# Optimization experiments

Hardware: AMD Instinct MI355X
Metric: run time of the kernel (lower is better)

The kernel has to match this reference:

```python
import jax, jax.numpy as jnp
import numpy as np

B = 2048
NUM_FEATURES = 40960
M = 256
N = 32
K = 32
MAX_EVAL = 10000.0  # Chess_Lib.MAX_EVAL stand-in
SPARSITY = 32.0 / NUM_FEATURES  # ~32 active HalfKP features per position


def _xavier(key, shape):
    fan_out, fan_in = shape
    limit = np.sqrt(6.0 / (fan_in + fan_out)).astype(np.float32)
    return jax.random.uniform(key, shape, jnp.float32, -limit, limit)


def setup_inputs() -> dict:
    key = jax.random.key(0)
    ks = jax.random.split(key, 8)
    # ~32-hot sparse binary feature vectors (HalfKP style)
    wf = (jax.random.uniform(ks[0], (B, NUM_FEATURES)) < SPARSITY).astype(jnp.float32)
    bf = (jax.random.uniform(ks[1], (B, NUM_FEATURES)) < SPARSITY).astype(jnp.float32)
    stm = jnp.round(jax.random.uniform(ks[2], (B, 1))).astype(jnp.float32)
    return {
        "white_features": wf,
        "black_features": bf,
        "stm": stm,
        "ft_w": _xavier(ks[3], (M, NUM_FEATURES)),
        "ft_b": jnp.zeros((M,), jnp.float32),
        "l1_w": _xavier(ks[4], (N, 2 * M)),
        "l1_b": jnp.zeros((N,), jnp.float32),
        "l2_w": _xavier(ks[5], (K, N)),
        "l2_b": jnp.zeros((K,), jnp.float32),
        "l3_w": _xavier(ks[6], (1, K)),
        "l3_b": jnp.zeros((1,), jnp.float32),
    }


def reference(white_features, black_features, stm, ft_w, ft_b,
              l1_w, l1_b, l2_w, l2_b, l3_w, l3_b):
    # feature transformer: [B,F] @ [F,M] -> [B,M]
    w = white_features @ ft_w.T + ft_b
    b = black_features @ ft_w.T + ft_b
    acc = stm * jnp.concatenate([w, b], axis=1) + (1.0 - stm) * jnp.concatenate([b, w], axis=1)
    l1_x = jnp.clip(acc, 0.0, 1.0)
    l2_x = jnp.clip(l1_x @ l1_w.T + l1_b, 0.0, 1.0)
    l3_x = jnp.clip(l2_x @ l2_w.T + l2_b, 0.0, 1.0)
    ev = jnp.clip(l3_x @ l3_w.T + l3_b, 0.0, 1.0)
    # align_eval without the python int() cast (kept batched/differentiable)
    return (ev - 0.5) * 2.0 * MAX_EVAL
```

## Files before the change

### kernel.cpp

```cpp
#include <hip/hip_runtime.h>
#include <hip/hip_bf16.h>

#define NF 40960
#define MD 256
#define BATCH 2048
#define NCHUNK 4
#define CHUNK (NF / NCHUNK)
#define CAPC 32

#define SCAN_BLOCKS (2 * BATCH * NCHUNK)
#define TRANS_BLOCKS ((NF / 64) * (MD / 64))

__device__ __forceinline__ float clip01(float v) {
    return fminf(fmaxf(v, 0.0f), 1.0f);
}

__global__ __launch_bounds__(256) void scan_transpose(
    const float* __restrict__ wf, const float* __restrict__ bfeat,
    const float* __restrict__ ft_w,
    float* __restrict__ ftT, int* __restrict__ g_cnt, int* __restrict__ g_idx)
{
    __shared__ float tile[64][65];
    __shared__ int s_cnt;
    __shared__ int s_idx[CAPC];

    const int b = blockIdx.x;
    const int t = threadIdx.x;

    if (b < SCAN_BLOCKS) {
        const int chunk = b & 3;
        const int pc    = b >> 2;
        const int color = pc & 1;
        const int pos   = pc >> 1;

        if (t == 0) s_cnt = 0;
        __syncthreads();

        const float* src = (color ? bfeat : wf) + (size_t)pos * NF + chunk * CHUNK;
        const float4* p4 = (const float4*)src;

        float4 v[10];
        #pragma unroll
        for (int k = 0; k < 10; ++k) v[k] = p4[t + 256 * k];

        #pragma unroll
        for (int k = 0; k < 10; ++k) {
            float4 a = v[k];
            if (a.x + a.y + a.z + a.w != 0.0f) {
                const int e = chunk * CHUNK + 4 * (t + 256 * k);
                if (a.x != 0.0f) { int q = atomicAdd(&s_cnt, 1); if (q < CAPC) s_idx[q] = e;     }
                if (a.y != 0.0f) { int q = atomicAdd(&s_cnt, 1); if (q < CAPC) s_idx[q] = e + 1; }
                if (a.z != 0.0f) { int q = atomicAdd(&s_cnt, 1); if (q < CAPC) s_idx[q] = e + 2; }
                if (a.w != 0.0f) { int q = atomicAdd(&s_cnt, 1); if (q < CAPC) s_idx[q] = e + 3; }
            }
        }
        __syncthreads();

        const int c = min(s_cnt, CAPC);
        if (t == 0) g_cnt[b] = c;
        if (t < c)  g_idx[(size_t)b * CAPC + t] = s_idx[t];
    } else {
        const int tb = b - SCAN_BLOCKS;
        const int f0 = (tb % (NF / 64)) * 64;
        const int m0 = (tb / (NF / 64)) * 64;
        const int tx = t & 63;
        const int ty = t >> 6;
        #pragma unroll
        for (int r = ty; r < 64; r += 4)
            tile[r][tx] = ft_w[(size_t)(m0 + r) * NF + f0 + tx];
        __syncthreads();
        #pragma unroll
        for (int r = ty; r < 64; r += 4)
            ftT[(size_t)(f0 + r) * MD + m0 + tx] = tile[tx][r];
    }
}

__global__ __launch_bounds__(256) void gather_mlp(
    const float* __restrict__ stm, const float* __restrict__ ftT,
    const int* __restrict__ g_cnt, const int* __restrict__ g_idx,
    const float* __restrict__ ft_b,
    const float* __restrict__ l1_w, const float* __restrict__ l1_b,
    const float* __restrict__ l2_w, const float* __restrict__ l2_b,
    const float* __restrict__ l3_w, const float* __restrict__ l3_b,
    float* __restrict__ out)
{
    __shared__ int lw[NCHUNK * CAPC], lb[NCHUNK * CAPC];
    __shared__ int cnts[8], offs[8];
    __shared__ int cw_s, cb_s;
    __shared__ float xsh[512];
    __shared__ float red[32][9];
    __shared__ float ysh[32], zsh[32];

    const int pos = blockIdx.x;
    const int t = threadIdx.x;

    if (t < 8) cnts[t] = g_cnt[(pos * 2 + (t >> 2)) * 4 + (t & 3)];
    __syncthreads();
    if (t == 0) {
        int ow = 0, ob = 0;
        #pragma unroll
        for (int c = 0; c < 4; ++c) {
            offs[c]     = ow; ow += cnts[c];
            offs[4 + c] = ob; ob += cnts[4 + c];
        }
        cw_s = ow; cb_s = ob;
    }
    __syncthreads();
    #pragma unroll
    for (int c = 0; c < 4; ++c) {
        if (t < cnts[c])     lw[offs[c] + t]     = g_idx[(size_t)((pos * 2 + 0) * 4 + c) * CAPC + t];
        if (t < cnts[4 + c]) lb[offs[4 + c] + t] = g_idx[(size_t)((pos * 2 + 1) * 4 + c) * CAPC + t];
    }
    __syncthreads();

    const int cw = cw_s, cb = cb_s;

    float accW = ft_b[t];
    float accB = ft_b[t];
    {
        int j = 0;
        for (; j + 4 <= cw; j += 4) {
            float a0 = ftT[(size_t)lw[j]     * MD + t];
            float a1 = ftT[(size_t)lw[j + 1] * MD + t];
            float a2 = ftT[(size_t)lw[j + 2] * MD + t];
            float a3 = ftT[(size_t)lw[j + 3] * MD + t];
            accW += a0 + a1 + a2 + a3;
        }
        for (; j < cw; ++j) accW += ftT[(size_t)lw[j] * MD + t];
        j = 0;
        for (; j + 4 <= cb; j += 4) {
            float a0 = ftT[(size_t)lb[j]     * MD + t];
            float a1 = ftT[(size_t)lb[j + 1] * MD + t];
            float a2 = ftT[(size_t)lb[j + 2] * MD + t];
            float a3 = ftT[(size_t)lb[j + 3] * MD + t];
            accB += a0 + a1 + a2 + a3;
        }
        for (; j < cb; ++j) accB += ftT[(size_t)lb[j] * MD + t];
    }

    const float s = stm[pos];
    xsh[t]       = clip01(s * accW + (1.0f - s) * accB);
    xsh[256 + t] = clip01(s * accB + (1.0f - s) * accW);
    __syncthreads();

    {
        const int n = t & 31;
        const int c = t >> 5;
        const float* w1 = l1_w + (size_t)n * 512 + c * 64;
        const float* xx = xsh + c * 64;
        float p = 0.0f;
        #pragma unroll
        for (int j = 0; j < 64; ++j) p += xx[j] * w1[j];
        red[n][c] = p;
    }
    __syncthreads();
    if (t < 32) {
        float v = l1_b[t];
        #pragma unroll
        for (int c = 0; c < 8; ++c) v += red[t][c];
        ysh[t] = clip01(v);
    }
    __syncthreads();

    if (t < 32) {
        float v = l2_b[t];
        const float* w2 = l2_w + t * 32;
        #pragma unroll
        for (int j = 0; j < 32; ++j) v += ysh[j] * w2[j];
        zsh[t] = clip01(v);
    }
    __syncthreads();

    if (t == 0) {
        float v = l3_b[0];
        #pragma unroll
        for (int j = 0; j < 32; ++j) v += zsh[j] * l3_w[j];
        v = clip01(v);
        out[pos] = (v - 0.5f) * 20000.0f;
    }
}

extern "C" void kernel_launch(void* const* d_in, const int* in_sizes, int n_in,
                              void* d_out, int out_size, void* d_ws, size_t ws_size,
                              hipStream_t stream) {
    const float* wf    = (const float*)d_in[0];
    const float* bfeat = (const float*)d_in[1];
    const float* stm   = (const float*)d_in[2];
    const float* ft_w  = (const float*)d_in[3];
    const float* ft_b  = (const float*)d_in[4];
    const float* l1_w  = (const float*)d_in[5];
    const float* l1_b  = (const float*)d_in[6];
    const float* l2_w  = (const float*)d_in[7];
    const float* l2_b  = (const float*)d_in[8];
    const float* l3_w  = (const float*)d_in[9];
    const float* l3_b  = (const float*)d_in[10];
    float* out = (float*)d_out;

    float* ftT   = (float*)d_ws;
    int*   g_cnt = (int*)((char*)d_ws + (size_t)NF * MD * sizeof(float));
    int*   g_idx = g_cnt + SCAN_BLOCKS;

    scan_transpose<<<SCAN_BLOCKS + TRANS_BLOCKS, 256, 0, stream>>>(
        wf, bfeat, ft_w, ftT, g_cnt, g_idx);

    gather_mlp<<<BATCH, 256, 0, stream>>>(
        stm, ftT, g_cnt, g_idx, ft_b,
        l1_w, l1_b, l2_w, l2_b, l3_w, l3_b, out);
}
```

Before: 698.9 us.

## Restructure feature scan per row with per-wave lists and vectorize gather

The scan now uses one block per feature row instead of four chunk blocks. Each wave keeps its own index list and counter, and a single atomicAdd reserves space for all nonzeros in a float4. Row loads are double-buffered so memory reads overlap the compaction work, and the transpose blocks are scheduled first. The gather uses float4 loads with the active-feature list split across four waves, then reduces the partial sums through shared memory. Together these aim to cut atomic contention and raise memory-level parallelism in the dominant dense input scan, at the cost of more registers and an extra shared-memory reduction step.

After: 710.8 us. No clear change (+1.7%).

```diff
diff --git a/kernel.cpp b/kernel.cpp
--- a/kernel.cpp
+++ b/kernel.cpp
@@ -4,12 +4,11 @@
 #define NF 40960
 #define MD 256
 #define BATCH 2048
-#define NCHUNK 4
-#define CHUNK (NF / NCHUNK)
-#define CAPC 32
-
-#define SCAN_BLOCKS (2 * BATCH * NCHUNK)
+#define ROWS (2 * BATCH)
+#define CAPW 48
+
 #define TRANS_BLOCKS ((NF / 64) * (MD / 64))
+#define SCAN_BLOCKS ROWS
 
 __device__ __forceinline__ float clip01(float v) {
     return fminf(fmaxf(v, 0.0f), 1.0f);
@@ -21,48 +20,15 @@
     float* __restrict__ ftT, int* __restrict__ g_cnt, int* __restrict__ g_idx)
 {
     __shared__ float tile[64][65];
-    __shared__ int s_cnt;
-    __shared__ int s_idx[CAPC];
+    __shared__ int s_cnt[4];
+    __shared__ int s_idx[4][CAPW];
 
     const int b = blockIdx.x;
     const int t = threadIdx.x;
 
-    if (b < SCAN_BLOCKS) {
-        const int chunk = b & 3;
-        const int pc    = b >> 2;
-        const int color = pc & 1;
-        const int pos   = pc >> 1;
-
-        if (t == 0) s_cnt = 0;
-        __syncthreads();
-
-        const float* src = (color ? bfeat : wf) + (size_t)pos * NF + chunk * CHUNK;
-        const float4* p4 = (const float4*)src;
-
-        float4 v[10];
-        #pragma unroll
-        for (int k = 0; k < 10; ++k) v[k] = p4[t + 256 * k];
-
-        #pragma unroll
-        for (int k = 0; k < 10; ++k) {
-            float4 a = v[k];
-            if (a.x + a.y + a.z + a.w != 0.0f) {
-                const int e = chunk * CHUNK + 4 * (t + 256 * k);
-                if (a.x != 0.0f) { int q = atomicAdd(&s_cnt, 1); if (q < CAPC) s_idx[q] = e;     }
-                if (a.y != 0.0f) { int q = atomicAdd(&s_cnt, 1); if (q < CAPC) s_idx[q] = e + 1; }
-                if (a.z != 0.0f) { int q = atomicAdd(&s_cnt, 1); if (q < CAPC) s_idx[q] = e + 2; }
-                if (a.w != 0.0f) { int q = atomicAdd(&s_cnt, 1); if (q < CAPC) s_idx[q] = e + 3; }
-            }
-        }
-        __syncthreads();
-
-        const int c = min(s_cnt, CAPC);
-        if (t == 0) g_cnt[b] = c;
-        if (t < c)  g_idx[(size_t)b * CAPC + t] = s_idx[t];
-    } else {
-        const int tb = b - SCAN_BLOCKS;
-        const int f0 = (tb % (NF / 64)) * 64;
-        const int m0 = (tb / (NF / 64)) * 64;
+    if (b < TRANS_BLOCKS) {
+        const int f0 = (b % (NF / 64)) * 64;
+        const int m0 = (b / (NF / 64)) * 64;
         const int tx = t & 63;
         const int ty = t >> 6;
         #pragma unroll
@@ -72,7 +38,50 @@
         #pragma unroll
         for (int r = ty; r < 64; r += 4)
             ftT[(size_t)(f0 + r) * MD + m0 + tx] = tile[tx][r];
-    }
+        return;
+    }
+
+    const int r     = b - TRANS_BLOCKS;
+    const int color = r & 1;
+    const int pos   = r >> 1;
+    const int w     = t >> 6;
+    const int lane  = t & 63;
+
+    if (lane == 0) s_cnt[w] = 0;
+
+    const float4* p4 = (const float4*)((color ? bfeat : wf) + (size_t)pos * NF);
+
+    float4 buf[2][4];
+    #pragma unroll
+    for (int i = 0; i < 4; ++i) buf[0][i] = p4[t + 256 * i];
+
+    #pragma unroll
+    for (int bb = 0; bb < 10; ++bb) {
+        const int cur = bb & 1, nxt = cur ^ 1;
+        if (bb < 9) {
+            #pragma unroll
+            for (int i = 0; i < 4; ++i)
+                buf[nxt][i] = p4[t + 256 * (4 * (bb + 1) + i)];
+        }
+        #pragma unroll
+        for (int i = 0; i < 4; ++i) {
+            float4 a = buf[cur][i];
+            if (a.x + a.y + a.z + a.w != 0.0f) {
+                const int nz = (a.x != 0.0f) + (a.y != 0.0f) +
+                               (a.z != 0.0f) + (a.w != 0.0f);
+                int q = atomicAdd(&s_cnt[w], nz);
+                const int col = 4 * (t + 256 * (4 * bb + i));
+                if (a.x != 0.0f) { if (q < CAPW) s_idx[w][q] = col;     ++q; }
+                if (a.y != 0.0f) { if (q < CAPW) s_idx[w][q] = col + 1; ++q; }
+                if (a.z != 0.0f) { if (q < CAPW) s_idx[w][q] = col + 2; ++q; }
+                if (a.w != 0.0f) { if (q < CAPW) s_idx[w][q] = col + 3; ++q; }
+            }
+        }
+    }
+
+    const int c = min(s_cnt[w], CAPW);
+    if (lane == 0) g_cnt[r * 4 + w] = c;
+    if (lane < c)  g_idx[(size_t)(r * 4 + w) * CAPW + lane] = s_idx[w][lane];
 }
 
 __global__ __launch_bounds__(256) void gather_mlp(
@@ -84,9 +93,11 @@
     const float* __restrict__ l3_w, const float* __restrict__ l3_b,
     float* __restrict__ out)
 {
-    __shared__ int lw[NCHUNK * CAPC], lb[NCHUNK * CAPC];
+    __shared__ int lw[4 * CAPW], lb[4 * CAPW];
     __shared__ int cnts[8], offs[8];
     __shared__ int cw_s, cb_s;
+    __shared__ float4 accw_sh[4][64];
+    __shared__ float4 accb_sh[4][64];
     __shared__ float xsh[512];
     __shared__ float red[32][9];
     __shared__ float ysh[32], zsh[32];
@@ -108,34 +119,55 @@
     __syncthreads();
     #pragma unroll
     for (int c = 0; c < 4; ++c) {
-        if (t < cnts[c])     lw[offs[c] + t]     = g_idx[(size_t)((pos * 2 + 0) * 4 + c) * CAPC + t];
-        if (t < cnts[4 + c]) lb[offs[4 + c] + t] = g_idx[(size_t)((pos * 2 + 1) * 4 + c) * CAPC + t];
+        if (t < cnts[c])     lw[offs[c] + t]     = g_idx[(size_t)((pos * 2 + 0) * 4 + c) * CAPW + t];
+        if (t < cnts[4 + c]) lb[offs[4 + c] + t] = g_idx[(size_t)((pos * 2 + 1) * 4 + c) * CAPW + t];
     }
     __syncthreads();
 
     const int cw = cw_s, cb = cb_s;
+    const int g  = t >> 6;
+    const int c4 = t & 63;
+
+    float4 a0 = {0.f, 0.f, 0.f, 0.f}, a1 = {0.f, 0.f, 0.f, 0.f};
+    {
+        int j = g;
+        for (; j + 4 < cw; j += 8) {
+            const float4 v0 = ((const float4*)(ftT + (size_t)lw[j]     * MD))[c4];
+            const float4 v1 = ((const float4*)(ftT + (size_t)lw[j + 4] * MD))[c4];
+            a0.x += v0.x; a0.y += v0.y; a0.z += v0.z; a0.w += v0.w;
+            a1.x += v1.x; a1.y += v1.y; a1.z += v1.z; a1.w += v1.w;
+        }
+        for (; j < cw; j += 4) {
+            const float4 v0 = ((const float4*)(ftT + (size_t)lw[j] * MD))[c4];
+            a0.x += v0.x; a0.y += v0.y; a0.z += v0.z; a0.w += v0.w;
+        }
+        a0.x += a1.x; a0.y += a1.y; a0.z += a1.z; a0.w += a1.w;
+        accw_sh[g][c4] = a0;
+    }
+    float4 b0 = {0.f, 0.f, 0.f, 0.f}, b1 = {0.f, 0.f, 0.f, 0.f};
+    {
+        int j = g;
+        for (; j + 4 < cb; j += 8) {
+            const float4 v0 = ((const float4*)(ftT + (size_t)lb[j]     * MD))[c4];
+            const float4 v1 = ((const float4*)(ftT + (size_t)lb[j + 4] * MD))[c4];
+            b0.x += v0.x; b0.y += v0.y; b0.z += v0.z; b0.w += v0.w;
+            b1.x += v1.x; b1.y += v1.y; b1.z += v1.z; b1.w += v1.w;
+        }
+        for (; j < cb; j += 4) {
+            const float4 v0 = ((const float4*)(ftT + (size_t)lb[j] * MD))[c4];
+            b0.x += v0.x; b0.y += v0.y; b0.z += v0.z; b0.w += v0.w;
+        }
+        b0.x += b1.x; b0.y += b1.y; b0.z += b1.z; b0.w += b1.w;
+        accb_sh[g][c4] = b0;
+    }
+    __syncthreads();
 
     float accW = ft_b[t];
     float accB = ft_b[t];
-    {
-        int j = 0;
-        for (; j + 4 <= cw; j += 4) {
-            float a0 = ftT[(size_t)lw[j]     * MD + t];
-            float a1 = ftT[(size_t)lw[j + 1] * MD + t];
-            float a2 = ftT[(size_t)lw[j + 2] * MD + t];
-            float a3 = ftT[(size_t)lw[j + 3] * MD + t];
-            accW += a0 + a1 + a2 + a3;
-        }
-        for (; j < cw; ++j) accW += ftT[(size_t)lw[j] * MD + t];
-        j = 0;
-        for (; j + 4 <= cb; j += 4) {
-            float a0 = ftT[(size_t)lb[j]     * MD + t];
-            float a1 = ftT[(size_t)lb[j + 1] * MD + t];
-            float a2 = ftT[(size_t)lb[j + 2] * MD + t];
-            float a3 = ftT[(size_t)lb[j + 3] * MD + t];
-            accB += a0 + a1 + a2 + a3;
-        }
-        for (; j < cb; ++j) accB += ftT[(size_t)lb[j] * MD + t];
+    #pragma unroll
+    for (int g2 = 0; g2 < 4; ++g2) {
+        accW += ((const float*)&accw_sh[g2][t >> 2])[t & 3];
+        accB += ((const float*)&accb_sh[g2][t >> 2])[t & 3];
     }
 
     const float s = stm[pos];
@@ -198,9 +230,9 @@
 
     float* ftT   = (float*)d_ws;
     int*   g_cnt = (int*)((char*)d_ws + (size_t)NF * MD * sizeof(float));
-    int*   g_idx = g_cnt + SCAN_BLOCKS;
-
-    scan_transpose<<<SCAN_BLOCKS + TRANS_BLOCKS, 256, 0, stream>>>(
+    int*   g_idx = g_cnt + ROWS * 4;
+
+    scan_transpose<<<TRANS_BLOCKS + SCAN_BLOCKS, 256, 0, stream>>>(
         wf, bfeat, ft_w, ftT, g_cnt, g_idx);
 
     gather_mlp<<<BATCH, 256, 0, stream>>>(
```
